# Kernel optimization log

Hardware: AMD Instinct MI355X
Metric: run time of the kernel (lower is better)

Reference implementation:

```python
import jax, jax.numpy as jnp
import numpy as np

EMBED_DIM = 512
PATCH = 16
QUANT_N = 1024
QUANT_DIM = 256
LN_EPS = 1e-5


def setup_inputs() -> dict:
    key = jax.random.key(0)
    k1, k2, k3, k4 = jax.random.split(key, 4)
    B, T, M = 16, 8192, 128
    fbank = jax.random.normal(k1, (B, T, M), dtype=jnp.float32)
    # xavier-normal conv weight (O,I,kH,kW), frozen in the original module
    fan = PATCH * PATCH + EMBED_DIM
    conv_w = jax.random.normal(k2, (EMBED_DIM, 1, PATCH, PATCH), dtype=jnp.float32) * np.sqrt(2.0 / fan)
    proj = jax.random.normal(k3, (EMBED_DIM, QUANT_DIM), dtype=jnp.float32) * np.sqrt(2.0 / (EMBED_DIM + QUANT_DIM))
    codebook = jax.random.normal(k4, (QUANT_N, QUANT_DIM), dtype=jnp.float32)
    return {"fbank": fbank, "conv_w": conv_w, "proj": proj, "codebook": codebook}


def _l2norm(x, eps=1e-12):
    return x / jnp.maximum(jnp.linalg.norm(x, axis=-1, keepdims=True), eps)


def reference(fbank, conv_w, proj, codebook):
    # patch embedding: Conv2d(1, D, k=16, s=16) over (B, 1, T, mel)
    x = fbank[:, None, :, :]  # B,1,T,M
    feats = jax.lax.conv_general_dilated(
        x, conv_w, window_strides=(PATCH, PATCH), padding='VALID',
        dimension_numbers=('NCHW', 'OIHW', 'NCHW'))  # B,D,T/16,M/16
    B, D, H, W = feats.shape
    feats = feats.reshape(B, D, H * W).transpose(0, 2, 1)  # B,N,D
    # LayerNorm without affine
    mu = jnp.mean(feats, axis=-1, keepdims=True)
    var = jnp.var(feats, axis=-1, keepdims=True)
    feats = (feats - mu) * jax.lax.rsqrt(var + LN_EPS)
    # random projection quantizer: l2norm(x @ P) vs l2-normalized codebook;
    # argmin euclidean distance == argmax cosine similarity for unit vectors
    p = _l2norm(jnp.einsum('bnd,dq->bnq', feats, proj))  # B,N,Q
    cb = _l2norm(codebook)                                # K,Q
    sim = jnp.einsum('bnq,kq->bnk', p, cb)                # B,N,K
    embed_ind = jnp.argmax(sim, axis=-1)                  # B,N int
    return embed_ind
```

## Files before the change

kernel.cpp:

```cpp
#include <hip/hip_runtime.h>
#include <math.h>

#define QD 256
#define QN 1024
#define TT 8192

typedef __bf16 bf16x8 __attribute__((ext_vector_type(8)));
typedef float  f32x16 __attribute__((ext_vector_type(16)));
typedef unsigned short ushort_t;
typedef unsigned short us8 __attribute__((ext_vector_type(8)));

#define PL  0
#define WS_ 49152
#define P1_ 50176
#define MU_ 51200
#define LM_ 53248
#define TN_ 53376
#define LX_ 54400
#define TH_ 55424
#define CN_ 55552
#define CC_ 55680
#define SMEM_TOTAL 59776

__device__ __forceinline__ void split3(float x, ushort_t& h, ushort_t& m, ushort_t& l) {
    unsigned int xu = __float_as_uint(x);
    h = (ushort_t)(xu >> 16);
    float hf = __uint_as_float(xu & 0xFFFF0000u);
    float r1 = x - hf;
    unsigned int r1u = __float_as_uint(r1);
    m = (ushort_t)(r1u >> 16);
    float mf = __uint_as_float(r1u & 0xFFFF0000u);
    float r2 = r1 - mf;
    l = (ushort_t)(__float_as_uint(r2) >> 16);
}
__device__ __forceinline__ f32x16 MF(bf16x8 a, bf16x8 b, f32x16 c) {
    return __builtin_amdgcn_mfma_f32_32x32x16_bf16(a, b, c, 0, 0, 0);
}

__global__ __launch_bounds__(256) void k_pre(const float* __restrict__ convw,
                                             const float* __restrict__ proj,
                                             const float* __restrict__ cb,
                                             ushort_t* __restrict__ cbph,
                                             float* __restrict__ cbn,
                                             ushort_t* __restrict__ w2p,
                                             float* __restrict__ wsum,
                                             float* __restrict__ p1) {
    int bx = blockIdx.x, t = threadIdx.x;
    if (bx < 256) {
        int c = bx*4 + (t>>6), lane = t&63;
        float4 v = ((const float4*)(cb + (size_t)c*QD))[lane];
        float ss = v.x*v.x + v.y*v.y + v.z*v.z + v.w*v.w;
        #pragma unroll
        for (int off = 32; off > 0; off >>= 1) ss += __shfl_down(ss, off);
        ss = __shfl(ss, 0);
        float inv = 1.0f/fmaxf(sqrtf(ss), 1e-12f);
        float4 vn = make_float4(v.x*inv, v.y*inv, v.z*inv, v.w*inv);
        *(float4*)(cbn + (size_t)c*QD + 4*lane) = vn;
        float vals[4] = {vn.x, vn.y, vn.z, vn.w};
        #pragma unroll
        for (int i = 0; i < 4; ++i) {
            int k = 4*lane + i;
            size_t base = ((size_t)(k>>4)*32 + (c>>5))*512 + (((k>>3)&1)*32 + (c&31))*8 + (k&7);
            cbph[base] = (ushort_t)(__float_as_uint(vals[i]) >> 16);
        }
    } else {
        int col = bx - 256;
        __shared__ float colv[512];
        if (col < 256) {
            const float* src = proj + col;
            colv[t]       = src[(size_t)t * 256];
            colv[t + 256] = src[(size_t)(t + 256) * 256];
            __syncthreads();
            float acc = 0.f;
            #pragma unroll 8
            for (int d = 0; d < 512; ++d) acc += convw[d*256 + t] * colv[d];
            ushort_t hb, mb, lb; split3(acc, hb, mb, lb);
            size_t base = ((size_t)(t>>4)*8 + (col>>5))*512 + (((t>>3)&1)*32 + (col&31))*8 + (t&7);
            w2p[base] = hb;
            w2p[base + 65536] = mb;
            w2p[base + 131072] = lb;
        } else if (col == 256) {
            float s = 0.f;
            #pragma unroll 8
            for (int d = 0; d < 512; ++d) s += convw[d*256 + t];
            wsum[t] = s;
        } else {
            float s = 0.f;
            #pragma unroll 8
            for (int d = 0; d < 512; ++d) s += proj[d*256 + t];
            p1[t] = s;
        }
    }
}

__global__ __launch_bounds__(512, 4) void k_mega(const float* __restrict__ fbank,
                                                 const ushort_t* __restrict__ w2p,
                                                 const ushort_t* __restrict__ cbph,
                                                 const float* __restrict__ cbn,
                                                 const float* __restrict__ wsum,
                                                 const float* __restrict__ p1,
                                                 int* __restrict__ out) {
    __shared__ char smem[SMEM_TOTAL];
    float* wsS   = (float*)(smem + WS_);
    float* p1S   = (float*)(smem + P1_);
    float* muS   = (float*)(smem + MU_);
    float* lnMuS = (float*)(smem + LM_);
    float* tn2P  = (float*)(smem + TN_);
    float* lmaxS = (float*)(smem + LX_);
    float* thrS  = (float*)(smem + TH_);
    int*   cntS  = (int*)(smem + CN_);
    ushort_t* candS = (ushort_t*)(smem + CC_);

    int tid = threadIdx.x;
    int n0 = blockIdx.x * 32;
    int w = tid >> 6, lane = tid & 63;
    int n31 = lane & 31, h = lane >> 5;
    size_t loff = (size_t)lane * 16;
    const char* w2pc = (const char*)w2p;
    const char* cbhc = (const char*)cbph;

    float4 va[2], vb[2];
    #pragma unroll
    for (int i = 0; i < 2; ++i) {
        int id = tid + 512*i;
        int kc = id >> 6, cl = id & 63;
        int tok = cl & 31, hh2 = cl >> 5;
        int n = n0 + tok;
        int b = n >> 12, r = n & 4095, th = r >> 3, wm = r & 7;
        const float* src = fbank + ((size_t)(b*TT + th*16 + kc))*128 + wm*16 + hh2*8;
        va[i] = ((const float4*)src)[0];
        vb[i] = ((const float4*)src)[1];
    }
    if (tid < 256) wsS[tid] = wsum[tid];
    else           p1S[tid - 256] = p1[tid - 256];
    __syncthreads();

    float mupart = 0.f;
    #pragma unroll
    for (int i = 0; i < 2; ++i) {
        int id = tid + 512*i;
        int kc = id >> 6, cl = id & 63;
        int hh2 = cl >> 5;
        float vals[8] = {va[i].x, va[i].y, va[i].z, va[i].w, vb[i].x, vb[i].y, vb[i].z, vb[i].w};
        us8 hv, mv, lv;
        #pragma unroll
        for (int j = 0; j < 8; ++j) {
            ushort_t a_, b_, c_; split3(vals[j], a_, b_, c_);
            hv[j] = a_; mv[j] = b_; lv[j] = c_;
            mupart += vals[j] * wsS[16*kc + 8*hh2 + j];
        }
        char* cp = smem + kc*1024 + cl*16;
        *(us8*)cp = hv;
        *(us8*)(cp + 16384) = mv;
        *(us8*)(cp + 32768) = lv;
    }
    muS[(tid>>5)*32 + (tid&31)] = mupart;
    __syncthreads();

    if (tid < 32) {
        float pm = 0.f;
        #pragma unroll
        for (int s = 0; s < 16; ++s) pm += muS[s*32 + tid];
        lnMuS[tid] = pm * (1.f/512.f);
    }

    f32x16 accE, accO;
    #pragma unroll
    for (int r2 = 0; r2 < 16; ++r2) { accE[r2] = 0.f; accO[r2] = 0.f; }
    for (int kc = 0; kc < 16; kc += 2) {
        bf16x8 a0[3], a1[3], b0[3], b1[3];
        #pragma unroll
        for (int q = 0; q < 3; ++q) {
            b0[q] = *(const bf16x8*)(w2pc + (size_t)q*131072 + (size_t)(kc*8 + w)*1024 + loff);
            b1[q] = *(const bf16x8*)(w2pc + (size_t)q*131072 + (size_t)((kc+1)*8 + w)*1024 + loff);
            a0[q] = *(const bf16x8*)(smem + q*16384 + kc*1024 + loff);
            a1[q] = *(const bf16x8*)(smem + q*16384 + (kc+1)*1024 + loff);
        }
        accE = MF(a0[0], b0[0], accE); accO = MF(a1[0], b1[0], accO);
        accE = MF(a0[0], b0[1], accE); accO = MF(a1[0], b1[1], accO);
        accE = MF(a0[1], b0[0], accE); accO = MF(a1[1], b1[0], accO);
        accE = MF(a0[1], b0[1], accE); accO = MF(a1[1], b1[1], accO);
        accE = MF(a0[0], b0[2], accE); accO = MF(a1[0], b1[2], accO);
        accE = MF(a0[2], b0[0], accE); accO = MF(a1[2], b1[0], accO);
    }
    __syncthreads();

    {
        int q = 32*w + n31;
        float p1v = p1S[q];
        #pragma unroll
        for (int reg = 0; reg < 16; ++reg) {
            int tok = (reg&3) + 8*(reg>>2) + 4*h;
            float tv = (accE[reg] + accO[reg]) - lnMuS[tok]*p1v;
            *(float*)(smem + 16384 + tok*1024 + q*4) = tv;
            *(ushort_t*)(smem + (q>>4)*1024 + (((q>>3)&1)*32 + tok)*16 + (q&7)*2)
                = (ushort_t)(__float_as_uint(tv) >> 16);
            float sq2 = tv*tv;
            #pragma unroll
            for (int msk = 1; msk < 32; msk <<= 1) sq2 += __shfl_xor(sq2, msk);
            if (n31 == 0) tn2P[tok*8 + w] = sq2;
        }
    }
    __syncthreads();

    f32x16 s0, s1, s2, s3;
    #pragma unroll
    for (int r2 = 0; r2 < 16; ++r2) { s0[r2]=0.f; s1[r2]=0.f; s2[r2]=0.f; s3[r2]=0.f; }
    for (int kc = 0; kc < 16; ++kc) {
        bf16x8 ah = *(const bf16x8*)(smem + kc*1024 + loff);
        bf16x8 q0 = *(const bf16x8*)(cbhc + (size_t)(kc*32 + w     )*1024 + loff);
        bf16x8 q1 = *(const bf16x8*)(cbhc + (size_t)(kc*32 + w + 8 )*1024 + loff);
        bf16x8 q2 = *(const bf16x8*)(cbhc + (size_t)(kc*32 + w + 16)*1024 + loff);
        bf16x8 q3 = *(const bf16x8*)(cbhc + (size_t)(kc*32 + w + 24)*1024 + loff);
        s0 = MF(ah, q0, s0); s1 = MF(ah, q1, s1);
        s2 = MF(ah, q2, s2); s3 = MF(ah, q3, s3);
    }
    #pragma unroll
    for (int reg = 0; reg < 16; ++reg) {
        int tok = (reg&3) + 8*(reg>>2) + 4*h;
        float m = fmaxf(fmaxf(s0[reg], s1[reg]), fmaxf(s2[reg], s3[reg]));
        #pragma unroll
        for (int msk = 1; msk < 32; msk <<= 1) m = fmaxf(m, __shfl_xor(m, msk));
        if (n31 == 0) lmaxS[tok*8 + w] = m;
    }
    __syncthreads();
    if (tid < 32) {
        float g = -3.4e38f, sq = 0.f;
        #pragma unroll
        for (int p = 0; p < 8; ++p) { g = fmaxf(g, lmaxS[tid*8 + p]); sq += tn2P[tid*8 + p]; }
        thrS[tid] = g - 0.04f*sqrtf(sq);
        cntS[tid] = 0;
    }
    __syncthreads();
    #pragma unroll
    for (int reg = 0; reg < 16; ++reg) {
        int tok = (reg&3) + 8*(reg>>2) + 4*h;
        float th_ = thrS[tok];
        if (s0[reg] >= th_) { int p = atomicAdd(&cntS[tok], 1); if (p < 64) candS[tok*64 + p] = (ushort_t)(32*(w     ) + n31); }
        if (s1[reg] >= th_) { int p = atomicAdd(&cntS[tok], 1); if (p < 64) candS[tok*64 + p] = (ushort_t)(32*(w + 8 ) + n31); }
        if (s2[reg] >= th_) { int p = atomicAdd(&cntS[tok], 1); if (p < 64) candS[tok*64 + p] = (ushort_t)(32*(w + 16) + n31); }
        if (s3[reg] >= th_) { int p = atomicAdd(&cntS[tok], 1); if (p < 64) candS[tok*64 + p] = (ushort_t)(32*(w + 24) + n31); }
    }
    __syncthreads();
    #pragma unroll
    for (int tk = 0; tk < 4; ++tk) {
        int tok = 4*w + tk;
        float4 tv = *(const float4*)(smem + 16384 + tok*1024 + lane*16);
        int nc = min(cntS[tok], 64);
        float bv = -3.4e38f; int bi = 0x7fffffff;
        for (int c = 0; c < nc; ++c) {
            int code = candS[tok*64 + c];
            float4 cv = *(const float4*)(cbn + (size_t)code*256 + 4*lane);
            float d = tv.x*cv.x + tv.y*cv.y + tv.z*cv.z + tv.w*cv.w;
            #pragma unroll
            for (int msk = 1; msk < 64; msk <<= 1) d += __shfl_xor(d, msk);
            if (d > bv || (d == bv && code < bi)) { bv = d; bi = code; }
        }
        if (lane == 0) out[n0 + tok] = bi;
    }
}

extern "C" void kernel_launch(void* const* d_in, const int* in_sizes, int n_in,
                              void* d_out, int out_size, void* d_ws, size_t ws_size,
                              hipStream_t stream) {
    const float* fbank = (const float*)d_in[0];
    const float* convw = (const float*)d_in[1];
    const float* proj  = (const float*)d_in[2];
    const float* cbook = (const float*)d_in[3];
    int* out = (int*)d_out;

    char* ws = (char*)d_ws;
    ushort_t* cbph = (ushort_t*)ws;
    float* cbn     = (float*)(ws + 0x080000);
    ushort_t* w2p  = (ushort_t*)(ws + 0x180000);
    float* wsum    = (float*)(ws + 0x1E0000);
    float* p1      = (float*)(ws + 0x1E1000);

    hipLaunchKernelGGL(k_pre,  dim3(514),  dim3(256), 0, stream,
                       convw, proj, cbook, cbph, cbn, w2p, wsum, p1);
    hipLaunchKernelGGL(k_mega, dim3(2048), dim3(512), 0, stream,
                       fbank, w2p, cbph, cbn, wsum, p1, out);
}
```

Before: 315.5 us.

## Software-pipeline global B-fragment loads and candidate rescoring; keep wsum/p1 in registers

Double-buffers the global loads of the projection and codebook MFMA fragments so the next k-chunk's loads are issued before the current chunk's MFMAs. The same prefetch is applied to the candidate rescoring loop, and wsum/p1 are read straight into registers instead of being staged through LDS behind a barrier. Prep-kernel reduction loops get a larger unroll. It also changes overflow handling: when more than 64 candidates pass the threshold, all 1024 codes are rescored instead of truncating, which improves correctness but can cost time on that path.

```diff
diff --git a/kernel.cpp b/kernel.cpp
--- a/kernel.cpp
+++ b/kernel.cpp
@@ -11,16 +11,14 @@
 typedef unsigned short us8 __attribute__((ext_vector_type(8)));
 
 #define PL  0
-#define WS_ 49152
-#define P1_ 50176
-#define MU_ 51200
-#define LM_ 53248
-#define TN_ 53376
-#define LX_ 54400
-#define TH_ 55424
-#define CN_ 55552
-#define CC_ 55680
-#define SMEM_TOTAL 59776
+#define MU_ 49152
+#define LM_ 51200
+#define TN_ 51328
+#define LX_ 52352
+#define TH_ 53376
+#define CN_ 53504
+#define CC_ 53632
+#define SMEM_TOTAL 57728
 
 __device__ __forceinline__ void split3(float x, ushort_t& h, ushort_t& m, ushort_t& l) {
     unsigned int xu = __float_as_uint(x);
@@ -72,7 +70,7 @@
             colv[t + 256] = src[(size_t)(t + 256) * 256];
             __syncthreads();
             float acc = 0.f;
-            #pragma unroll 8
+            #pragma unroll 32
             for (int d = 0; d < 512; ++d) acc += convw[d*256 + t] * colv[d];
             ushort_t hb, mb, lb; split3(acc, hb, mb, lb);
             size_t base = ((size_t)(t>>4)*8 + (col>>5))*512 + (((t>>3)&1)*32 + (col&31))*8 + (t&7);
@@ -81,12 +79,12 @@
             w2p[base + 131072] = lb;
         } else if (col == 256) {
             float s = 0.f;
-            #pragma unroll 8
+            #pragma unroll 32
             for (int d = 0; d < 512; ++d) s += convw[d*256 + t];
             wsum[t] = s;
         } else {
             float s = 0.f;
-            #pragma unroll 8
+            #pragma unroll 32
             for (int d = 0; d < 512; ++d) s += proj[d*256 + t];
             p1[t] = s;
         }
@@ -101,8 +99,6 @@
                                                  const float* __restrict__ p1,
                                                  int* __restrict__ out) {
     __shared__ char smem[SMEM_TOTAL];
-    float* wsS   = (float*)(smem + WS_);
-    float* p1S   = (float*)(smem + P1_);
     float* muS   = (float*)(smem + MU_);
     float* lnMuS = (float*)(smem + LM_);
     float* tn2P  = (float*)(smem + TN_);
@@ -118,6 +114,31 @@
     size_t loff = (size_t)lane * 16;
     const char* w2pc = (const char*)w2p;
     const char* cbhc = (const char*)cbph;
+
+    auto loadB1 = [&](int kcv, bf16x8 (&dst)[3]) {
+        #pragma unroll
+        for (int q = 0; q < 3; ++q)
+            dst[q] = *(const bf16x8*)(w2pc + (size_t)q*131072 + (size_t)(kcv*8 + w)*1024 + loff);
+    };
+    auto loadB2 = [&](int kcv, bf16x8 (&dst)[4]) {
+        dst[0] = *(const bf16x8*)(cbhc + (size_t)(kcv*32 + w     )*1024 + loff);
+        dst[1] = *(const bf16x8*)(cbhc + (size_t)(kcv*32 + w + 8 )*1024 + loff);
+        dst[2] = *(const bf16x8*)(cbhc + (size_t)(kcv*32 + w + 16)*1024 + loff);
+        dst[3] = *(const bf16x8*)(cbhc + (size_t)(kcv*32 + w + 24)*1024 + loff);
+    };
+    auto loadA = [&](int kcv, bf16x8 (&a)[3]) {
+        #pragma unroll
+        for (int p = 0; p < 3; ++p)
+            a[p] = *(const bf16x8*)(smem + p*16384 + kcv*1024 + loff);
+    };
+    auto compute6 = [&](bf16x8 (&a)[3], bf16x8 (&b)[3], f32x16& acc) {
+        acc = MF(a[0], b[0], acc);
+        acc = MF(a[0], b[1], acc);
+        acc = MF(a[1], b[0], acc);
+        acc = MF(a[1], b[1], acc);
+        acc = MF(a[0], b[2], acc);
+        acc = MF(a[2], b[0], acc);
+    };
 
     float4 va[2], vb[2];
     #pragma unroll
@@ -131,23 +152,35 @@
         va[i] = ((const float4*)src)[0];
         vb[i] = ((const float4*)src)[1];
     }
-    if (tid < 256) wsS[tid] = wsum[tid];
-    else           p1S[tid - 256] = p1[tid - 256];
-    __syncthreads();
+    int kc0 = tid >> 6, hh0 = (tid >> 5) & 1;
+    int wb0 = 16*kc0 + 8*hh0;
+    float4 w00 = *(const float4*)(wsum + wb0);
+    float4 w01 = *(const float4*)(wsum + wb0 + 4);
+    float4 w10 = *(const float4*)(wsum + wb0 + 128);
+    float4 w11 = *(const float4*)(wsum + wb0 + 132);
+    float p1v = p1[32*w + n31];
+
+    bf16x8 bA[3], bB[3];
+    loadB1(0, bA);
+
+    float wsv[2][8];
+    wsv[0][0]=w00.x; wsv[0][1]=w00.y; wsv[0][2]=w00.z; wsv[0][3]=w00.w;
+    wsv[0][4]=w01.x; wsv[0][5]=w01.y; wsv[0][6]=w01.z; wsv[0][7]=w01.w;
+    wsv[1][0]=w10.x; wsv[1][1]=w10.y; wsv[1][2]=w10.z; wsv[1][3]=w10.w;
+    wsv[1][4]=w11.x; wsv[1][5]=w11.y; wsv[1][6]=w11.z; wsv[1][7]=w11.w;
 
     float mupart = 0.f;
     #pragma unroll
     for (int i = 0; i < 2; ++i) {
         int id = tid + 512*i;
         int kc = id >> 6, cl = id & 63;
-        int hh2 = cl >> 5;
         float vals[8] = {va[i].x, va[i].y, va[i].z, va[i].w, vb[i].x, vb[i].y, vb[i].z, vb[i].w};
         us8 hv, mv, lv;
         #pragma unroll
         for (int j = 0; j < 8; ++j) {
             ushort_t a_, b_, c_; split3(vals[j], a_, b_, c_);
             hv[j] = a_; mv[j] = b_; lv[j] = c_;
-            mupart += vals[j] * wsS[16*kc + 8*hh2 + j];
+            mupart += vals[j] * wsv[i][j];
         }
         char* cp = smem + kc*1024 + cl*16;
         *(us8*)cp = hv;
@@ -168,26 +201,19 @@
     #pragma unroll
     for (int r2 = 0; r2 < 16; ++r2) { accE[r2] = 0.f; accO[r2] = 0.f; }
     for (int kc = 0; kc < 16; kc += 2) {
-        bf16x8 a0[3], a1[3], b0[3], b1[3];
-        #pragma unroll
-        for (int q = 0; q < 3; ++q) {
-            b0[q] = *(const bf16x8*)(w2pc + (size_t)q*131072 + (size_t)(kc*8 + w)*1024 + loff);
-            b1[q] = *(const bf16x8*)(w2pc + (size_t)q*131072 + (size_t)((kc+1)*8 + w)*1024 + loff);
-            a0[q] = *(const bf16x8*)(smem + q*16384 + kc*1024 + loff);
-            a1[q] = *(const bf16x8*)(smem + q*16384 + (kc+1)*1024 + loff);
-        }
-        accE = MF(a0[0], b0[0], accE); accO = MF(a1[0], b1[0], accO);
-        accE = MF(a0[0], b0[1], accE); accO = MF(a1[0], b1[1], accO);
-        accE = MF(a0[1], b0[0], accE); accO = MF(a1[1], b1[0], accO);
-        accE = MF(a0[1], b0[1], accE); accO = MF(a1[1], b1[1], accO);
-        accE = MF(a0[0], b0[2], accE); accO = MF(a1[0], b1[2], accO);
-        accE = MF(a0[2], b0[0], accE); accO = MF(a1[2], b1[0], accO);
-    }
+        loadB1(kc + 1, bB);
+        { bf16x8 a[3]; loadA(kc, a); compute6(a, bA, accE); }
+        if (kc + 2 < 16) loadB1(kc + 2, bA);
+        { bf16x8 a[3]; loadA(kc + 1, a); compute6(a, bB, accO); }
+    }
+
+    bf16x8 qA[4], qB[4];
+    loadB2(0, qA);
+
     __syncthreads();
 
     {
         int q = 32*w + n31;
-        float p1v = p1S[q];
         #pragma unroll
         for (int reg = 0; reg < 16; ++reg) {
             int tok = (reg&3) + 8*(reg>>2) + 4*h;
@@ -206,14 +232,19 @@
     f32x16 s0, s1, s2, s3;
     #pragma unroll
     for (int r2 = 0; r2 < 16; ++r2) { s0[r2]=0.f; s1[r2]=0.f; s2[r2]=0.f; s3[r2]=0.f; }
-    for (int kc = 0; kc < 16; ++kc) {
-        bf16x8 ah = *(const bf16x8*)(smem + kc*1024 + loff);
-        bf16x8 q0 = *(const bf16x8*)(cbhc + (size_t)(kc*32 + w     )*1024 + loff);
-        bf16x8 q1 = *(const bf16x8*)(cbhc + (size_t)(kc*32 + w + 8 )*1024 + loff);
-        bf16x8 q2 = *(const bf16x8*)(cbhc + (size_t)(kc*32 + w + 16)*1024 + loff);
-        bf16x8 q3 = *(const bf16x8*)(cbhc + (size_t)(kc*32 + w + 24)*1024 + loff);
-        s0 = MF(ah, q0, s0); s1 = MF(ah, q1, s1);
-        s2 = MF(ah, q2, s2); s3 = MF(ah, q3, s3);
+    for (int kc = 0; kc < 16; kc += 2) {
+        loadB2(kc + 1, qB);
+        {
+            bf16x8 ah = *(const bf16x8*)(smem + kc*1024 + loff);
+            s0 = MF(ah, qA[0], s0); s1 = MF(ah, qA[1], s1);
+            s2 = MF(ah, qA[2], s2); s3 = MF(ah, qA[3], s3);
+        }
+        if (kc + 2 < 16) loadB2(kc + 2, qA);
+        {
+            bf16x8 ah = *(const bf16x8*)(smem + (kc+1)*1024 + loff);
+            s0 = MF(ah, qB[0], s0); s1 = MF(ah, qB[1], s1);
+            s2 = MF(ah, qB[2], s2); s3 = MF(ah, qB[3], s3);
+        }
     }
     #pragma unroll
     for (int reg = 0; reg < 16; ++reg) {
@@ -242,19 +273,28 @@
         if (s3[reg] >= th_) { int p = atomicAdd(&cntS[tok], 1); if (p < 64) candS[tok*64 + p] = (ushort_t)(32*(w + 24) + n31); }
     }
     __syncthreads();
-    #pragma unroll
+    #pragma unroll 1
     for (int tk = 0; tk < 4; ++tk) {
         int tok = 4*w + tk;
         float4 tv = *(const float4*)(smem + 16384 + tok*1024 + lane*16);
-        int nc = min(cntS[tok], 64);
+        int nc = cntS[tok];
+        bool full = (nc > 64);
+        if (full) nc = 1024;
         float bv = -3.4e38f; int bi = 0x7fffffff;
+        int code = full ? 0 : candS[tok*64];
+        float4 cv = *(const float4*)(cbn + (size_t)code*256 + 4*lane);
         for (int c = 0; c < nc; ++c) {
-            int code = candS[tok*64 + c];
-            float4 cv = *(const float4*)(cbn + (size_t)code*256 + 4*lane);
-            float d = tv.x*cv.x + tv.y*cv.y + tv.z*cv.z + tv.w*cv.w;
+            int ncode = code;
+            float4 nv = cv;
+            if (c + 1 < nc) {
+                ncode = full ? (c + 1) : (int)candS[tok*64 + c + 1];
+                nv = *(const float4*)(cbn + (size_t)ncode*256 + 4*lane);
+            }
+            float d = cv.x*tv.x + cv.y*tv.y + cv.z*tv.z + cv.w*tv.w;
             #pragma unroll
             for (int msk = 1; msk < 64; msk <<= 1) d += __shfl_xor(d, msk);
             if (d > bv || (d == bv && code < bi)) { bv = d; bi = code; }
+            code = ncode; cv = nv;
         }
         if (lane == 0) out[n0 + tok] = bi;
     }
```

Result: no change. 316.5 us (+0.3%).
